# Kernel optimization log

Hardware: AMD Instinct MI355X
Metric: run time of the kernel (lower is better)

## Reference

```python
import jax, jax.numpy as jnp
import numpy as np

DIM = 128
HID = 256
NB = 2048      # number of sets (batches)
NTOT = 32768   # total elements across all sets
NMAX = 32      # cap on decoded set size (padded/masked)
VAL_MID = (DIM + HID) // 2    # 192, build_mlp midmult=1.0
SIZE_MID = (HID + 1) // 2     # 128
DEC_MID = (HID + DIM) // 2    # 192


def mish(x):
    return x * jnp.tanh(jax.nn.softplus(x))


def layernorm(x, g, b):
    m = x.mean(-1, keepdims=True)
    v = x.var(-1, keepdims=True)
    return (x - m) / jnp.sqrt(v + 1e-5) * g + b


def _lin_init(key, fan_in, fan_out):
    return jax.random.normal(key, (fan_in, fan_out), jnp.float32) / np.sqrt(fan_in)


def setup_inputs() -> dict:
    key = jax.random.key(0)
    ks = jax.random.split(key, 16)
    x = jax.random.normal(ks[0], (NTOT, DIM), jnp.float32)
    batch = jnp.sort(jax.random.randint(ks[1], (NTOT,), 0, NB)).astype(jnp.int64)
    return {
        "x": x, "batch": batch,
        # encoder rank (Linear(dim,1))
        "rank_w": _lin_init(ks[2], DIM, 1)[:, 0], "rank_b": jnp.zeros((), jnp.float32),
        # encoder val_net: Linear -> LayerNorm -> Mish -> Linear
        "val_w1": _lin_init(ks[3], DIM, VAL_MID), "val_b1": jnp.zeros((VAL_MID,), jnp.float32),
        "val_ln_g": jnp.ones((VAL_MID,), jnp.float32), "val_ln_b": jnp.zeros((VAL_MID,), jnp.float32),
        "val_w2": _lin_init(ks[4], VAL_MID, HID), "val_b2": jnp.zeros((HID,), jnp.float32),
        # shared cardinality Linear(1, hidden)
        "card_w": _lin_init(ks[5], 1, HID), "card_b": jnp.zeros((HID,), jnp.float32),
        # decoder size_pred: Linear -> LayerNorm -> Mish -> Linear
        "size_w1": _lin_init(ks[6], HID, SIZE_MID), "size_b1": jnp.zeros((SIZE_MID,), jnp.float32),
        "size_ln_g": jnp.ones((SIZE_MID,), jnp.float32), "size_ln_b": jnp.zeros((SIZE_MID,), jnp.float32),
        "size_w2": _lin_init(ks[7], SIZE_MID, 1), "size_b2": jnp.zeros((1,), jnp.float32),
        # decoder mlp: Linear -> Mish -> Linear (no layernorm)
        "dec_w1": _lin_init(ks[8], HID, DEC_MID), "dec_b1": jnp.zeros((DEC_MID,), jnp.float32),
        "dec_w2": _lin_init(ks[9], DEC_MID, DIM), "dec_b2": jnp.zeros((DIM,), jnp.float32),
    }


def reference(x, batch, rank_w, rank_b, val_w1, val_b1, val_ln_g, val_ln_b,
              val_w2, val_b2, card_w, card_b, size_w1, size_b1, size_ln_g,
              size_ln_b, size_w2, size_b2, dec_w1, dec_b1, dec_w2, dec_b2):
    batch = batch.astype(jnp.int32)
    t = jnp.linspace(0.0, 1.0, HID)

    # ---- encoder ----
    n = jax.ops.segment_sum(jnp.ones((NTOT,), jnp.float32), batch, num_segments=NB)
    n_i = n.astype(jnp.int32)
    mag = x @ rank_w + rank_b                       # [NTOT]
    # sort within each contiguous batch segment: stable lexsort (batch primary)
    order = jnp.lexsort((mag, batch))
    xs = x[order]
    seg_start = jnp.cumsum(n_i) - n_i               # per-set start offset
    k = (jnp.arange(NTOT, dtype=jnp.int32) - seg_start[batch]).astype(jnp.float32)
    keys = jnp.exp(1j * t[None, :] * k[:, None] * 8.0)            # [NTOT,HID] complex
    h = mish(layernorm(xs @ val_w1 + val_b1, val_ln_g, val_ln_b)) @ val_w2 + val_b2
    y = h.astype(jnp.complex64) * keys
    z_el = jax.ops.segment_sum(y, batch, num_segments=NB)         # [NB,HID] complex
    n_enc = n[:, None] @ card_w + card_b
    z = z_el + n_enc

    # ---- decoder ----
    h2 = mish(layernorm(z.real @ size_w1 + size_b1, size_ln_g, size_ln_b)) @ size_w2 + size_b2
    n_pred = jnp.maximum(jnp.round(h2[:, 0]), 0.0)                # [NB]
    n_pred_i = jnp.minimum(n_pred.astype(jnp.int32), NMAX)
    n_enc2 = n_pred[:, None] @ card_w + card_b
    zc = z - n_enc2
    kk = jnp.arange(NMAX, dtype=jnp.float32)
    keys2 = jnp.exp(1j * t[None, :] * kk[:, None] * 8.0)          # [NMAX,HID]
    zp = zc[:, None, :] * keys2[None, :, :]                       # [NB,NMAX,HID] complex
    xr = mish(zp.real @ dec_w1 + dec_b1) @ dec_w2 + dec_b2        # [NB,NMAX,DIM]
    mask = jnp.arange(NMAX)[None, :] < n_pred_i[:, None]          # [NB,NMAX]
    xr = jnp.where(mask[:, :, None], xr, 0.0)
    return xr, mask, n_pred_i
```

## Files before the change

### kernel.cpp

```cpp
#include <hip/hip_runtime.h>
#include <math.h>

#define DIMX 128
#define HIDX 256
#define NBX 2048
#define NTOTX 32768
#define NMAXX 32
#define VMID 192
#define SMID 128
#define DMID 192

#define EROWS 64
#define SP 68
#define NSEGMAX 128

__device__ __forceinline__ float mishf(float v) {
    if (v > 20.0f) return v;
    float u = expf(v);
    float t = u * (u + 2.0f);
    return v * (t / (t + 2.0f));
}

__global__ void k_wt(const float* __restrict__ w1, const float* __restrict__ w2,
                     float* __restrict__ wI1, float* __restrict__ wI2) {
    int i = blockIdx.x * blockDim.x + threadIdx.x;
    if (i < DIMX * VMID) {
        int k = i / VMID, c = i % VMID;
        wI1[((k >> 2) * VMID + c) * 4 + (k & 3)] = w1[i];
    }
    int i2 = i - DIMX * VMID;
    if (i2 >= 0 && i2 < VMID * HIDX) {
        int k = i2 / HIDX, c = i2 % HIDX;
        wI2[((k >> 2) * HIDX + c) * 4 + (k & 3)] = w2[i2];
    }
}

__global__ __launch_bounds__(512, 4) void k_enc(const float* __restrict__ x,
    const float* __restrict__ rw, const float* __restrict__ rb,
    const float4* __restrict__ wI1, const float* __restrict__ b1,
    const float* __restrict__ g1, const float* __restrict__ be1,
    const float4* __restrict__ wI2, const float* __restrict__ b2,
    float* __restrict__ h, float* __restrict__ mag) {
    __shared__ __align__(16) float sT[VMID * SP];
    int tid = threadIdx.x;
    int rowbase = blockIdx.x * EROWS;

#pragma unroll
    for (int it = 0; it < 4; it++) {
        int idx = it * 512 + tid;
        int r = idx >> 5, kq = idx & 31;
        float4 v = ((const float4*)x)[(size_t)(rowbase + r) * 32 + kq];
        sT[(4 * kq + 0) * SP + r] = v.x;
        sT[(4 * kq + 1) * SP + r] = v.y;
        sT[(4 * kq + 2) * SP + r] = v.z;
        sT[(4 * kq + 3) * SP + r] = v.w;
    }
    __syncthreads();

    if (tid < EROWS) {
        float s = 0.0f;
        for (int k = 0; k < DIMX; k++) s += sT[k * SP + tid] * rw[k];
        mag[rowbase + tid] = s + rb[0];
    }

    int c = tid & 63;
    int rg = tid >> 6;
    int r0 = rg * 8;

    float a0[8], a1[8], a2[8];
#pragma unroll
    for (int i = 0; i < 8; i++) { a0[i] = 0.f; a1[i] = 0.f; a2[i] = 0.f; }
    const float4* w1g = wI1 + c;
#pragma unroll 4
    for (int kg = 0; kg < DIMX / 4; kg++) {
        float4 wa = w1g[kg * VMID];
        float4 wb = w1g[kg * VMID + 64];
        float4 wc = w1g[kg * VMID + 128];
        const float waA[4] = {wa.x, wa.y, wa.z, wa.w};
        const float wbA[4] = {wb.x, wb.y, wb.z, wb.w};
        const float wcA[4] = {wc.x, wc.y, wc.z, wc.w};
#pragma unroll
        for (int kk = 0; kk < 4; kk++) {
            const float4* xp = (const float4*)&sT[(4 * kg + kk) * SP + r0];
            float4 t0 = xp[0], t1 = xp[1];
            float xv[8] = {t0.x, t0.y, t0.z, t0.w, t1.x, t1.y, t1.z, t1.w};
#pragma unroll
            for (int i = 0; i < 8; i++) {
                a0[i] += waA[kk] * xv[i];
                a1[i] += wbA[kk] * xv[i];
                a2[i] += wcA[kk] * xv[i];
            }
        }
    }

    float b1a = b1[c], b1b = b1[c + 64], b1c = b1[c + 128];
    float g1a = g1[c], g1b = g1[c + 64], g1c = g1[c + 128];
    float e1a = be1[c], e1b = be1[c + 64], e1c = be1[c + 128];
#pragma unroll
    for (int i = 0; i < 8; i++) {
        float v0 = a0[i] + b1a, v1 = a1[i] + b1b, v2 = a2[i] + b1c;
        float s = v0 + v1 + v2;
#pragma unroll
        for (int off = 32; off; off >>= 1) s += __shfl_xor(s, off, 64);
        float mean = s / 192.0f;
        float d0 = v0 - mean, d1 = v1 - mean, d2 = v2 - mean;
        float q = d0 * d0 + d1 * d1 + d2 * d2;
#pragma unroll
        for (int off = 32; off; off >>= 1) q += __shfl_xor(q, off, 64);
        float inv = 1.0f / sqrtf(q / 192.0f + 1e-5f);
        a0[i] = mishf(d0 * inv * g1a + e1a);
        a1[i] = mishf(d1 * inv * g1b + e1b);
        a2[i] = mishf(d2 * inv * g1c + e1c);
    }
    __syncthreads();
#pragma unroll
    for (int i = 0; i < 8; i++) {
        sT[c * SP + r0 + i]          = a0[i];
        sT[(c + 64) * SP + r0 + i]   = a1[i];
        sT[(c + 128) * SP + r0 + i]  = a2[i];
    }
    __syncthreads();

    float c0[8], c1[8], c2[8], c3[8];
#pragma unroll
    for (int i = 0; i < 8; i++) { c0[i] = 0.f; c1[i] = 0.f; c2[i] = 0.f; c3[i] = 0.f; }
    const float4* w2g = wI2 + c;
#pragma unroll 4
    for (int kg = 0; kg < VMID / 4; kg++) {
        float4 wa = w2g[kg * HIDX];
        float4 wb = w2g[kg * HIDX + 64];
        float4 wc = w2g[kg * HIDX + 128];
        float4 wd = w2g[kg * HIDX + 192];
        const float waA[4] = {wa.x, wa.y, wa.z, wa.w};
        const float wbA[4] = {wb.x, wb.y, wb.z, wb.w};
        const float wcA[4] = {wc.x, wc.y, wc.z, wc.w};
        const float wdA[4] = {wd.x, wd.y, wd.z, wd.w};
#pragma unroll
        for (int kk = 0; kk < 4; kk++) {
            const float4* ap = (const float4*)&sT[(4 * kg + kk) * SP + r0];
            float4 t0 = ap[0], t1 = ap[1];
            float av[8] = {t0.x, t0.y, t0.z, t0.w, t1.x, t1.y, t1.z, t1.w};
#pragma unroll
            for (int i = 0; i < 8; i++) {
                c0[i] += waA[kk] * av[i];
                c1[i] += wbA[kk] * av[i];
                c2[i] += wcA[kk] * av[i];
                c3[i] += wdA[kk] * av[i];
            }
        }
    }
    float b2a = b2[c], b2b = b2[c + 64], b2c = b2[c + 128], b2d = b2[c + 192];
#pragma unroll
    for (int i = 0; i < 8; i++) {
        size_t row = (size_t)(rowbase + r0 + i);
        h[row * HIDX + c]        = c0[i] + b2a;
        h[row * HIDX + c + 64]   = c1[i] + b2b;
        h[row * HIDX + c + 128]  = c2[i] + b2c;
        h[row * HIDX + c + 192]  = c3[i] + b2d;
    }
}

__global__ __launch_bounds__(256) void k_z(const float* __restrict__ h,
    const int* __restrict__ batch, const float* __restrict__ mag,
    const float* __restrict__ cw, const float* __restrict__ cb,
    const float* __restrict__ sw1, const float* __restrict__ sb1,
    const float* __restrict__ sg, const float* __restrict__ sbe,
    const float* __restrict__ sw2, const float* __restrict__ sb2,
    float* __restrict__ zcre, float* __restrict__ zim,
    float* __restrict__ out_mask, float* __restrict__ out_np,
    int* __restrict__ npredi) {
    __shared__ float zrow[HIDX];
    __shared__ float magL[NSEGMAX];
    __shared__ int   ordL[NSEGMAX];
    __shared__ int   shs, shn;
    __shared__ float red0[2], red1[2], red2[2];
    int b = blockIdx.x, j = threadIdx.x;
    if (j == 0) {
        int lo = 0, hi = NTOTX;
        while (lo < hi) { int m = (lo + hi) >> 1; if (batch[m] < b) lo = m + 1; else hi = m; }
        int stt = lo;
        hi = NTOTX;
        while (lo < hi) { int m = (lo + hi) >> 1; if (batch[m] <= b) lo = m + 1; else hi = m; }
        shs = stt; shn = lo - stt;
    }
    __syncthreads();
    int s = shs, n_true = shn;
    int n = (n_true < NSEGMAX) ? n_true : NSEGMAX;
    if (j < n) magL[j] = mag[s + j];
    __syncthreads();
    if (j < n) {
        float mi = magL[j];
        int rk = 0;
        for (int q = 0; q < n; q++) {
            float mq = magL[q];
            rk += (mq < mi) || (mq == mi && q < j);
        }
        ordL[rk] = s + j;
    }
    __syncthreads();

    float t = (float)j * (1.0f / 255.0f);
    float zr = 0.f, zi = 0.f;
    int p = 0;
    for (; p + 1 < n; p += 2) {
        int e0 = ordL[p], e1 = ordL[p + 1];
        float hv0 = h[(size_t)e0 * HIDX + j];
        float hv1 = h[(size_t)e1 * HIDX + j];
        float sv0, cv0, sv1, cv1;
        sincosf((t * (float)p) * 8.0f, &sv0, &cv0);
        sincosf((t * (float)(p + 1)) * 8.0f, &sv1, &cv1);
        zr += hv0 * cv0; zi += hv0 * sv0;
        zr += hv1 * cv1; zi += hv1 * sv1;
    }
    if (p < n) {
        int e = ordL[p];
        float hv = h[(size_t)e * HIDX + j];
        float sv, cv;
        sincosf((t * (float)p) * 8.0f, &sv, &cv);
        zr += hv * cv; zi += hv * sv;
    }
    float nf = (float)n_true;
    float zrev = zr + nf * cw[j] + cb[j];
    zrow[j] = zrev;
    zim[(size_t)b * HIDX + j] = zi;
    __syncthreads();

    float v = 0.0f;
    if (j < SMID) {
        v = sb1[j];
        for (int k = 0; k < HIDX; k++) v += zrow[k] * sw1[k * SMID + j];
    }
    float sa = v;
#pragma unroll
    for (int off = 32; off; off >>= 1) sa += __shfl_xor(sa, off, 64);
    if (j < SMID && (j & 63) == 0) red0[j >> 6] = sa;
    __syncthreads();
    float mean = (red0[0] + red0[1]) / 128.0f;
    float d = v - mean;
    float q2 = d * d;
#pragma unroll
    for (int off = 32; off; off >>= 1) q2 += __shfl_xor(q2, off, 64);
    if (j < SMID && (j & 63) == 0) red1[j >> 6] = q2;
    __syncthreads();
    float var = (red1[0] + red1[1]) / 128.0f;
    float p2 = 0.0f;
    if (j < SMID) {
        float lv = d * (1.0f / sqrtf(var + 1e-5f)) * sg[j] + sbe[j];
        p2 = mishf(lv) * sw2[j];
    }
#pragma unroll
    for (int off = 32; off; off >>= 1) p2 += __shfl_xor(p2, off, 64);
    if (j < SMID && (j & 63) == 0) red2[j >> 6] = p2;
    __syncthreads();
    float h2 = red2[0] + red2[1] + sb2[0];
    float npf = fmaxf(rintf(h2), 0.0f);
    int npi = min((int)npf, NMAXX);
    zcre[(size_t)b * HIDX + j] = zrow[j] - (npf * cw[j] + cb[j]);
    if (j < NMAXX) out_mask[b * NMAXX + j] = (j < npi) ? 1.0f : 0.0f;
    if (j == 0) { out_np[b] = (float)npi; npredi[b] = npi; }
}

__global__ __launch_bounds__(256) void k_dec(const float* __restrict__ zcre,
    const float* __restrict__ zim, const int* __restrict__ npredi,
    const float* __restrict__ w1, const float* __restrict__ b1,
    const float* __restrict__ w2, const float* __restrict__ b2,
    float* __restrict__ xr) {
    int m = blockIdx.x, b = blockIdx.y;
    int tid = threadIdx.x;
    size_t row = (size_t)b * NMAXX + m;
    if (m >= npredi[b]) {
        if (tid < DIMX) xr[row * DIMX + tid] = 0.0f;
        return;
    }
    __shared__ float zp[HIDX];
    __shared__ float a[DMID];
    {
        float t = (float)tid * (1.0f / 255.0f);
        float sv, cv;
        sincosf((t * (float)m) * 8.0f, &sv, &cv);
        zp[tid] = zcre[(size_t)b * HIDX + tid] * cv - zim[(size_t)b * HIDX + tid] * sv;
    }
    __syncthreads();
    if (tid < DMID) {
        float v = b1[tid];
#pragma unroll 4
        for (int k = 0; k < HIDX; k++) v += zp[k] * w1[k * DMID + tid];
        a[tid] = mishf(v);
    }
    __syncthreads();
    if (tid < DIMX) {
        float v = b2[tid];
#pragma unroll 4
        for (int k = 0; k < DMID; k++) v += a[k] * w2[k * DIMX + tid];
        xr[row * DIMX + tid] = v;
    }
}

extern "C" void kernel_launch(void* const* d_in, const int* in_sizes, int n_in,
                              void* d_out, int out_size, void* d_ws, size_t ws_size,
                              hipStream_t stream) {
    const float* x      = (const float*)d_in[0];
    const int*   batch  = (const int*)d_in[1];
    const float* rank_w = (const float*)d_in[2];
    const float* rank_b = (const float*)d_in[3];
    const float* vw1    = (const float*)d_in[4];
    const float* vb1    = (const float*)d_in[5];
    const float* vlg    = (const float*)d_in[6];
    const float* vlb    = (const float*)d_in[7];
    const float* vw2    = (const float*)d_in[8];
    const float* vb2    = (const float*)d_in[9];
    const float* cw     = (const float*)d_in[10];
    const float* cb     = (const float*)d_in[11];
    const float* sw1    = (const float*)d_in[12];
    const float* sb1    = (const float*)d_in[13];
    const float* slg    = (const float*)d_in[14];
    const float* slb    = (const float*)d_in[15];
    const float* sw2    = (const float*)d_in[16];
    const float* sb2    = (const float*)d_in[17];
    const float* dw1    = (const float*)d_in[18];
    const float* db1    = (const float*)d_in[19];
    const float* dw2    = (const float*)d_in[20];
    const float* db2    = (const float*)d_in[21];

    char* ws = (char*)d_ws;
    size_t off = 0;
    auto alloc = [&](size_t bytes) {
        void* p = ws + off;
        off += (bytes + 255) & ~(size_t)255;
        return p;
    };
    float* mag  = (float*)alloc((size_t)NTOTX * 4);
    float* zim  = (float*)alloc((size_t)NBX * HIDX * 4);
    float* zcre = (float*)alloc((size_t)NBX * HIDX * 4);
    int*   npi  = (int*)alloc((size_t)NBX * 4);
    float* wI1  = (float*)alloc((size_t)DIMX * VMID * 4);
    float* wI2  = (float*)alloc((size_t)VMID * HIDX * 4);
    float* h    = (float*)alloc((size_t)NTOTX * HIDX * 4);

    float* out_xr   = (float*)d_out;
    float* out_mask = out_xr + (size_t)NBX * NMAXX * DIMX;
    float* out_np   = out_mask + (size_t)NBX * NMAXX;

    hipLaunchKernelGGL(k_wt,   dim3((DIMX * VMID + VMID * HIDX + 255) / 256), dim3(256), 0, stream,
                       vw1, vw2, wI1, wI2);
    hipLaunchKernelGGL(k_enc,  dim3(NTOTX / EROWS), dim3(512), 0, stream,
                       x, rank_w, rank_b, (const float4*)wI1, vb1, vlg, vlb,
                       (const float4*)wI2, vb2, h, mag);
    hipLaunchKernelGGL(k_z,    dim3(NBX), dim3(HIDX), 0, stream,
                       h, batch, mag, cw, cb,
                       sw1, sb1, slg, slb, sw2, sb2,
                       zcre, zim, out_mask, out_np, npi);
    hipLaunchKernelGGL(k_dec,  dim3(NMAXX, NBX), dim3(256), 0, stream,
                       zcre, zim, npi, dw1, db1, dw2, db2, out_xr);
    (void)in_sizes; (void)n_in; (void)out_size; (void)ws_size;
}
```

Measured before the change: 157.2 us.

## Enlarge encoder per-thread register tile and interleave weight layout for contiguous columns

The encoder MLP kernel drops from 512 to 256 threads per block, and each thread now computes 6 (first layer) or 8 (second layer) contiguous output columns for 8 rows instead of 3 or 4 strided ones. Weights are re-laid out so each thread's column group loads as float4s, and the h output is written as float4 vectors. The goal is more FMAs per shared-memory load and wider global stores. In exchange, register pressure rises (up to 64 accumulators), which may lower occupancy or cause spills, and the LayerNorm reduction shrinks to 32-lane shuffles.

After: 161.4 us. +2.7%, slower.

```diff
diff --git a/kernel.cpp b/kernel.cpp
--- a/kernel.cpp
+++ b/kernel.cpp
@@ -26,16 +26,18 @@
     int i = blockIdx.x * blockDim.x + threadIdx.x;
     if (i < DIMX * VMID) {
         int k = i / VMID, c = i % VMID;
-        wI1[((k >> 2) * VMID + c) * 4 + (k & 3)] = w1[i];
+        int kg = k >> 2, kk = k & 3, cg = c / 6, j = c % 6;
+        wI1[(((kg * 6 + j) * 32) + cg) * 4 + kk] = w1[i];
     }
     int i2 = i - DIMX * VMID;
     if (i2 >= 0 && i2 < VMID * HIDX) {
         int k = i2 / HIDX, c = i2 % HIDX;
-        wI2[((k >> 2) * HIDX + c) * 4 + (k & 3)] = w2[i2];
-    }
-}
-
-__global__ __launch_bounds__(512, 4) void k_enc(const float* __restrict__ x,
+        int kg = k >> 2, kk = k & 3, cg = c >> 3, j = c & 7;
+        wI2[(((kg * 8 + j) * 32) + cg) * 4 + kk] = w2[i2];
+    }
+}
+
+__global__ __launch_bounds__(256, 2) void k_enc(const float* __restrict__ x,
     const float* __restrict__ rw, const float* __restrict__ rb,
     const float4* __restrict__ wI1, const float* __restrict__ b1,
     const float* __restrict__ g1, const float* __restrict__ be1,
@@ -46,8 +48,8 @@
     int rowbase = blockIdx.x * EROWS;
 
 #pragma unroll
-    for (int it = 0; it < 4; it++) {
-        int idx = it * 512 + tid;
+    for (int it = 0; it < 8; it++) {
+        int idx = it * 256 + tid;
         int r = idx >> 5, kq = idx & 31;
         float4 v = ((const float4*)x)[(size_t)(rowbase + r) * 32 + kq];
         sT[(4 * kq + 0) * SP + r] = v.x;
@@ -63,100 +65,105 @@
         mag[rowbase + tid] = s + rb[0];
     }
 
-    int c = tid & 63;
-    int rg = tid >> 6;
+    int cg = tid & 31;
+    int rg = tid >> 5;
     int r0 = rg * 8;
 
-    float a0[8], a1[8], a2[8];
-#pragma unroll
-    for (int i = 0; i < 8; i++) { a0[i] = 0.f; a1[i] = 0.f; a2[i] = 0.f; }
-    const float4* w1g = wI1 + c;
-#pragma unroll 4
+    float acc[6][8];
+#pragma unroll
+    for (int j = 0; j < 6; j++)
+#pragma unroll
+        for (int i = 0; i < 8; i++) acc[j][i] = 0.0f;
+    const float4* w1p = wI1 + cg;
+#pragma unroll 2
     for (int kg = 0; kg < DIMX / 4; kg++) {
-        float4 wa = w1g[kg * VMID];
-        float4 wb = w1g[kg * VMID + 64];
-        float4 wc = w1g[kg * VMID + 128];
-        const float waA[4] = {wa.x, wa.y, wa.z, wa.w};
-        const float wbA[4] = {wb.x, wb.y, wb.z, wb.w};
-        const float wcA[4] = {wc.x, wc.y, wc.z, wc.w};
+        float4 wv[6];
+#pragma unroll
+        for (int j = 0; j < 6; j++) wv[j] = w1p[(kg * 6 + j) * 32];
 #pragma unroll
         for (int kk = 0; kk < 4; kk++) {
             const float4* xp = (const float4*)&sT[(4 * kg + kk) * SP + r0];
             float4 t0 = xp[0], t1 = xp[1];
             float xv[8] = {t0.x, t0.y, t0.z, t0.w, t1.x, t1.y, t1.z, t1.w};
 #pragma unroll
-            for (int i = 0; i < 8; i++) {
-                a0[i] += waA[kk] * xv[i];
-                a1[i] += wbA[kk] * xv[i];
-                a2[i] += wcA[kk] * xv[i];
+            for (int j = 0; j < 6; j++) {
+                float w = ((const float*)&wv[j])[kk];
+#pragma unroll
+                for (int i = 0; i < 8; i++) acc[j][i] += w * xv[i];
             }
         }
     }
 
-    float b1a = b1[c], b1b = b1[c + 64], b1c = b1[c + 128];
-    float g1a = g1[c], g1b = g1[c + 64], g1c = g1[c + 128];
-    float e1a = be1[c], e1b = be1[c + 64], e1c = be1[c + 128];
+    float b1v[6], g1v[6], e1v[6];
+#pragma unroll
+    for (int j = 0; j < 6; j++) {
+        b1v[j] = b1[cg * 6 + j];
+        g1v[j] = g1[cg * 6 + j];
+        e1v[j] = be1[cg * 6 + j];
+    }
 #pragma unroll
     for (int i = 0; i < 8; i++) {
-        float v0 = a0[i] + b1a, v1 = a1[i] + b1b, v2 = a2[i] + b1c;
-        float s = v0 + v1 + v2;
-#pragma unroll
-        for (int off = 32; off; off >>= 1) s += __shfl_xor(s, off, 64);
-        float mean = s / 192.0f;
-        float d0 = v0 - mean, d1 = v1 - mean, d2 = v2 - mean;
-        float q = d0 * d0 + d1 * d1 + d2 * d2;
-#pragma unroll
-        for (int off = 32; off; off >>= 1) q += __shfl_xor(q, off, 64);
-        float inv = 1.0f / sqrtf(q / 192.0f + 1e-5f);
-        a0[i] = mishf(d0 * inv * g1a + e1a);
-        a1[i] = mishf(d1 * inv * g1b + e1b);
-        a2[i] = mishf(d2 * inv * g1c + e1c);
-    }
-    __syncthreads();
-#pragma unroll
-    for (int i = 0; i < 8; i++) {
-        sT[c * SP + r0 + i]          = a0[i];
-        sT[(c + 64) * SP + r0 + i]   = a1[i];
-        sT[(c + 128) * SP + r0 + i]  = a2[i];
-    }
-    __syncthreads();
-
-    float c0[8], c1[8], c2[8], c3[8];
-#pragma unroll
-    for (int i = 0; i < 8; i++) { c0[i] = 0.f; c1[i] = 0.f; c2[i] = 0.f; c3[i] = 0.f; }
-    const float4* w2g = wI2 + c;
-#pragma unroll 4
+        float s = 0.0f;
+#pragma unroll
+        for (int j = 0; j < 6; j++) { acc[j][i] += b1v[j]; s += acc[j][i]; }
+#pragma unroll
+        for (int off = 16; off; off >>= 1) s += __shfl_xor(s, off, 64);
+        float mean = s * (1.0f / 192.0f);
+        float q = 0.0f;
+#pragma unroll
+        for (int j = 0; j < 6; j++) {
+            acc[j][i] -= mean;
+            q += acc[j][i] * acc[j][i];
+        }
+#pragma unroll
+        for (int off = 16; off; off >>= 1) q += __shfl_xor(q, off, 64);
+        float inv = 1.0f / sqrtf(q * (1.0f / 192.0f) + 1e-5f);
+#pragma unroll
+        for (int j = 0; j < 6; j++)
+            acc[j][i] = mishf(acc[j][i] * inv * g1v[j] + e1v[j]);
+    }
+    __syncthreads();
+#pragma unroll
+    for (int j = 0; j < 6; j++)
+#pragma unroll
+        for (int i = 0; i < 8; i++)
+            sT[(cg * 6 + j) * SP + r0 + i] = acc[j][i];
+    __syncthreads();
+
+    float c2[8][8];
+#pragma unroll
+    for (int j = 0; j < 8; j++)
+#pragma unroll
+        for (int i = 0; i < 8; i++) c2[j][i] = 0.0f;
+    const float4* w2p = wI2 + cg;
+#pragma unroll 2
     for (int kg = 0; kg < VMID / 4; kg++) {
-        float4 wa = w2g[kg * HIDX];
-        float4 wb = w2g[kg * HIDX + 64];
-        float4 wc = w2g[kg * HIDX + 128];
-        float4 wd = w2g[kg * HIDX + 192];
-        const float waA[4] = {wa.x, wa.y, wa.z, wa.w};
-        const float wbA[4] = {wb.x, wb.y, wb.z, wb.w};
-        const float wcA[4] = {wc.x, wc.y, wc.z, wc.w};
-        const float wdA[4] = {wd.x, wd.y, wd.z, wd.w};
+        float4 wv[8];
+#pragma unroll
+        for (int j = 0; j < 8; j++) wv[j] = w2p[(kg * 8 + j) * 32];
 #pragma unroll
         for (int kk = 0; kk < 4; kk++) {
             const float4* ap = (const float4*)&sT[(4 * kg + kk) * SP + r0];
             float4 t0 = ap[0], t1 = ap[1];
             float av[8] = {t0.x, t0.y, t0.z, t0.w, t1.x, t1.y, t1.z, t1.w};
 #pragma unroll
-            for (int i = 0; i < 8; i++) {
-                c0[i] += waA[kk] * av[i];
-                c1[i] += wbA[kk] * av[i];
-                c2[i] += wcA[kk] * av[i];
-                c3[i] += wdA[kk] * av[i];
+            for (int j = 0; j < 8; j++) {
+                float w = ((const float*)&wv[j])[kk];
+#pragma unroll
+                for (int i = 0; i < 8; i++) c2[j][i] += w * av[i];
             }
         }
     }
-    float b2a = b2[c], b2b = b2[c + 64], b2c = b2[c + 128], b2d = b2[c + 192];
+    float b2v[8];
+#pragma unroll
+    for (int j = 0; j < 8; j++) b2v[j] = b2[cg * 8 + j];
 #pragma unroll
     for (int i = 0; i < 8; i++) {
-        size_t row = (size_t)(rowbase + r0 + i);
-        h[row * HIDX + c]        = c0[i] + b2a;
-        h[row * HIDX + c + 64]   = c1[i] + b2b;
-        h[row * HIDX + c + 128]  = c2[i] + b2c;
-        h[row * HIDX + c + 192]  = c3[i] + b2d;
+        float* hp = h + (size_t)(rowbase + r0 + i) * HIDX + cg * 8;
+        float4 v0 = {c2[0][i] + b2v[0], c2[1][i] + b2v[1], c2[2][i] + b2v[2], c2[3][i] + b2v[3]};
+        float4 v1 = {c2[4][i] + b2v[4], c2[5][i] + b2v[5], c2[6][i] + b2v[6], c2[7][i] + b2v[7]};
+        ((float4*)hp)[0] = v0;
+        ((float4*)hp)[1] = v1;
     }
 }
 
@@ -343,7 +350,7 @@
 
     hipLaunchKernelGGL(k_wt,   dim3((DIMX * VMID + VMID * HIDX + 255) / 256), dim3(256), 0, stream,
                        vw1, vw2, wI1, wI2);
-    hipLaunchKernelGGL(k_enc,  dim3(NTOTX / EROWS), dim3(512), 0, stream,
+    hipLaunchKernelGGL(k_enc,  dim3(NTOTX / EROWS), dim3(256), 0, stream,
                        x, rank_w, rank_b, (const float4*)wI1, vb1, vlg, vlb,
                        (const float4*)wI2, vb2, h, mag);
     hipLaunchKernelGGL(k_z,    dim3(NBX), dim3(HIDX), 0, stream,
```

## Compact decoder work into atomic worklist and zero padded rows in k_z

Applied to the files above, without the earlier changes.

k_z now appends each valid (set, slot) pair to a global worklist through an atomic counter and writes the zero padding of xr itself. k_dec becomes a persistent grid-stride kernel over that list, so it no longer launches 65536 blocks where most exit early. The encoder's shared-memory pad also changes from 68 to 66, with float2 reads replacing float4 reads, to reduce LDS bank conflicts. The risks are the atomic's nondeterministic output order, serial list writes by thread 0, and narrower LDS loads.

After: 160.2 us. No clear change (+2.0%).

```diff
diff --git a/kernel.cpp b/kernel.cpp
--- a/kernel.cpp
+++ b/kernel.cpp
@@ -11,7 +11,7 @@
 #define DMID 192
 
 #define EROWS 64
-#define SP 68
+#define SP 66
 #define NSEGMAX 128
 
 __device__ __forceinline__ float mishf(float v) {
@@ -22,8 +22,10 @@
 }
 
 __global__ void k_wt(const float* __restrict__ w1, const float* __restrict__ w2,
-                     float* __restrict__ wI1, float* __restrict__ wI2) {
+                     float* __restrict__ wI1, float* __restrict__ wI2,
+                     int* __restrict__ wcount) {
     int i = blockIdx.x * blockDim.x + threadIdx.x;
+    if (i == 0) wcount[0] = 0;
     if (i < DIMX * VMID) {
         int k = i / VMID, c = i % VMID;
         wI1[((k >> 2) * VMID + c) * 4 + (k & 3)] = w1[i];
@@ -81,9 +83,9 @@
         const float wcA[4] = {wc.x, wc.y, wc.z, wc.w};
 #pragma unroll
         for (int kk = 0; kk < 4; kk++) {
-            const float4* xp = (const float4*)&sT[(4 * kg + kk) * SP + r0];
-            float4 t0 = xp[0], t1 = xp[1];
-            float xv[8] = {t0.x, t0.y, t0.z, t0.w, t1.x, t1.y, t1.z, t1.w};
+            const float2* xp = (const float2*)&sT[(4 * kg + kk) * SP + r0];
+            float2 t0 = xp[0], t1 = xp[1], t2 = xp[2], t3 = xp[3];
+            float xv[8] = {t0.x, t0.y, t1.x, t1.y, t2.x, t2.y, t3.x, t3.y};
 #pragma unroll
             for (int i = 0; i < 8; i++) {
                 a0[i] += waA[kk] * xv[i];
@@ -137,9 +139,9 @@
         const float wdA[4] = {wd.x, wd.y, wd.z, wd.w};
 #pragma unroll
         for (int kk = 0; kk < 4; kk++) {
-            const float4* ap = (const float4*)&sT[(4 * kg + kk) * SP + r0];
-            float4 t0 = ap[0], t1 = ap[1];
-            float av[8] = {t0.x, t0.y, t0.z, t0.w, t1.x, t1.y, t1.z, t1.w};
+            const float2* ap = (const float2*)&sT[(4 * kg + kk) * SP + r0];
+            float2 t0 = ap[0], t1 = ap[1], t2 = ap[2], t3 = ap[3];
+            float av[8] = {t0.x, t0.y, t1.x, t1.y, t2.x, t2.y, t3.x, t3.y};
 #pragma unroll
             for (int i = 0; i < 8; i++) {
                 c0[i] += waA[kk] * av[i];
@@ -168,12 +170,13 @@
     const float* __restrict__ sw2, const float* __restrict__ sb2,
     float* __restrict__ zcre, float* __restrict__ zim,
     float* __restrict__ out_mask, float* __restrict__ out_np,
-    int* __restrict__ npredi) {
+    float* __restrict__ xr, int* __restrict__ wcount, int* __restrict__ wlist) {
     __shared__ float zrow[HIDX];
     __shared__ float magL[NSEGMAX];
     __shared__ int   ordL[NSEGMAX];
     __shared__ int   shs, shn;
     __shared__ float red0[2], red1[2], red2[2];
+    __shared__ int   snpi;
     int b = blockIdx.x, j = threadIdx.x;
     if (j == 0) {
         int lo = 0, hi = NTOTX;
@@ -257,42 +260,55 @@
     int npi = min((int)npf, NMAXX);
     zcre[(size_t)b * HIDX + j] = zrow[j] - (npf * cw[j] + cb[j]);
     if (j < NMAXX) out_mask[b * NMAXX + j] = (j < npi) ? 1.0f : 0.0f;
-    if (j == 0) { out_np[b] = (float)npi; npredi[b] = npi; }
+    if (j == 0) {
+        out_np[b] = (float)npi;
+        snpi = npi;
+        int base = atomicAdd(wcount, npi);
+        for (int m = 0; m < npi; m++) wlist[base + m] = (b << 5) | m;
+    }
+    __syncthreads();
+    {
+        int npi2 = snpi;
+        float4* base4 = (float4*)(xr + (size_t)b * NMAXX * DIMX);
+        for (int idx = npi2 * 32 + j; idx < NMAXX * 32; idx += 256)
+            base4[idx] = make_float4(0.f, 0.f, 0.f, 0.f);
+    }
 }
 
 __global__ __launch_bounds__(256) void k_dec(const float* __restrict__ zcre,
-    const float* __restrict__ zim, const int* __restrict__ npredi,
+    const float* __restrict__ zim, const int* __restrict__ wcount,
+    const int* __restrict__ wlist,
     const float* __restrict__ w1, const float* __restrict__ b1,
     const float* __restrict__ w2, const float* __restrict__ b2,
     float* __restrict__ xr) {
-    int m = blockIdx.x, b = blockIdx.y;
-    int tid = threadIdx.x;
-    size_t row = (size_t)b * NMAXX + m;
-    if (m >= npredi[b]) {
-        if (tid < DIMX) xr[row * DIMX + tid] = 0.0f;
-        return;
-    }
     __shared__ float zp[HIDX];
     __shared__ float a[DMID];
-    {
-        float t = (float)tid * (1.0f / 255.0f);
-        float sv, cv;
-        sincosf((t * (float)m) * 8.0f, &sv, &cv);
-        zp[tid] = zcre[(size_t)b * HIDX + tid] * cv - zim[(size_t)b * HIDX + tid] * sv;
-    }
-    __syncthreads();
-    if (tid < DMID) {
-        float v = b1[tid];
+    int tid = threadIdx.x;
+    int count = *wcount;
+    for (int it = blockIdx.x; it < count; it += gridDim.x) {
+        int wv = wlist[it];
+        int b = wv >> 5, m = wv & 31;
+        {
+            float t = (float)tid * (1.0f / 255.0f);
+            float sv, cv;
+            sincosf((t * (float)m) * 8.0f, &sv, &cv);
+            zp[tid] = zcre[(size_t)b * HIDX + tid] * cv - zim[(size_t)b * HIDX + tid] * sv;
+        }
+        __syncthreads();
+        if (tid < DMID) {
+            float v = b1[tid];
 #pragma unroll 4
-        for (int k = 0; k < HIDX; k++) v += zp[k] * w1[k * DMID + tid];
-        a[tid] = mishf(v);
-    }
-    __syncthreads();
-    if (tid < DIMX) {
-        float v = b2[tid];
+            for (int k = 0; k < HIDX; k++) v += zp[k] * w1[k * DMID + tid];
+            a[tid] = mishf(v);
+        }
+        __syncthreads();
+        if (tid < DIMX) {
+            float v = b2[tid];
 #pragma unroll 4
-        for (int k = 0; k < DMID; k++) v += a[k] * w2[k * DIMX + tid];
-        xr[row * DIMX + tid] = v;
+            for (int k = 0; k < DMID; k++) v += a[k] * w2[k * DIMX + tid];
+            xr[((size_t)b * NMAXX + m) * DIMX + tid] = v;
+        }
+        __syncthreads();
     }
 }
 
@@ -329,28 +345,29 @@
         off += (bytes + 255) & ~(size_t)255;
         return p;
     };
-    float* mag  = (float*)alloc((size_t)NTOTX * 4);
-    float* zim  = (float*)alloc((size_t)NBX * HIDX * 4);
-    float* zcre = (float*)alloc((size_t)NBX * HIDX * 4);
-    int*   npi  = (int*)alloc((size_t)NBX * 4);
-    float* wI1  = (float*)alloc((size_t)DIMX * VMID * 4);
-    float* wI2  = (float*)alloc((size_t)VMID * HIDX * 4);
-    float* h    = (float*)alloc((size_t)NTOTX * HIDX * 4);
+    float* mag    = (float*)alloc((size_t)NTOTX * 4);
+    float* zim    = (float*)alloc((size_t)NBX * HIDX * 4);
+    float* zcre   = (float*)alloc((size_t)NBX * HIDX * 4);
+    int*   wcount = (int*)alloc(256);
+    int*   wlist  = (int*)alloc((size_t)NBX * NMAXX * 4);
+    float* wI1    = (float*)alloc((size_t)DIMX * VMID * 4);
+    float* wI2    = (float*)alloc((size_t)VMID * HIDX * 4);
+    float* h      = (float*)alloc((size_t)NTOTX * HIDX * 4);
 
     float* out_xr   = (float*)d_out;
     float* out_mask = out_xr + (size_t)NBX * NMAXX * DIMX;
     float* out_np   = out_mask + (size_t)NBX * NMAXX;
 
     hipLaunchKernelGGL(k_wt,   dim3((DIMX * VMID + VMID * HIDX + 255) / 256), dim3(256), 0, stream,
-                       vw1, vw2, wI1, wI2);
+                       vw1, vw2, wI1, wI2, wcount);
     hipLaunchKernelGGL(k_enc,  dim3(NTOTX / EROWS), dim3(512), 0, stream,
                        x, rank_w, rank_b, (const float4*)wI1, vb1, vlg, vlb,
                        (const float4*)wI2, vb2, h, mag);
     hipLaunchKernelGGL(k_z,    dim3(NBX), dim3(HIDX), 0, stream,
                        h, batch, mag, cw, cb,
                        sw1, sb1, slg, slb, sw2, sb2,
-                       zcre, zim, out_mask, out_np, npi);
-    hipLaunchKernelGGL(k_dec,  dim3(NMAXX, NBX), dim3(256), 0, stream,
-                       zcre, zim, npi, dw1, db1, dw2, db2, out_xr);
+                       zcre, zim, out_mask, out_np, out_xr, wcount, wlist);
+    hipLaunchKernelGGL(k_dec,  dim3(2048), dim3(256), 0, stream,
+                       zcre, zim, wcount, wlist, dw1, db1, dw2, db2, out_xr);
     (void)in_sizes; (void)n_in; (void)out_size; (void)ws_size;
 }
```
